# Kernel optimization log

Hardware: AMD Instinct MI355X
Metric: run time of the kernel (lower is better)

The kernel has to match this reference:

```python
import jax, jax.numpy as jnp
import numpy as np

EPS = 1e-12  # torch F.normalize eps

def _l2norm(x, axis):
    n = jnp.sqrt(jnp.sum(x * x, axis=axis, keepdims=True))
    return x / jnp.maximum(n, EPS)

def setup_inputs() -> dict:
    key = jax.random.key(0)
    k1, k2, k3, k4 = jax.random.split(key, 4)
    B, Lq, Ld, D, NWAY = 128, 32, 180, 128, 8
    query_reps = jax.random.normal(k1, (B, Lq, D), dtype=jnp.float32)
    doc_reps = jax.random.normal(k2, (B, NWAY, Ld, D), dtype=jnp.float32)
    doc_mask = jax.random.randint(k3, (B, NWAY, Ld), 0, 2, dtype=jnp.int32)
    # labels are teacher log-probabilities (KLDivLoss log_target=True)
    labels = jax.nn.log_softmax(jax.random.normal(k4, (B, NWAY), dtype=jnp.float32), axis=-1)
    return {"query_reps": query_reps, "doc_reps": doc_reps, "doc_mask": doc_mask, "labels": labels}

def reference(query_reps, doc_reps, doc_mask, labels):
    # query: L2-normalize over feature dim (dim=2 in torch call)
    q = _l2norm(query_reps, axis=-1)                      # [B, Lq, D]
    # docs: mask padding tokens, then F.normalize with DEFAULT dim=1,
    # i.e. L2-normalize along the token axis (faithful to source).
    d = doc_reps * doc_mask[..., None].astype(doc_reps.dtype)  # [B, W, Ld, D]
    d = _l2norm(d, axis=2)
    # MaxSim: sim[b,w,q,l] = <q_bq, d_bwl>; max over doc tokens, sum over query tokens
    sim = jnp.einsum('bqd,bwld->bwql', q, d)              # [B, W, Lq, Ld]
    scores = jnp.max(sim, axis=-1).sum(axis=-1)           # [B, W]
    log_p = jax.nn.log_softmax(scores, axis=-1)           # == log(softmax(scores))
    # KLDivLoss(log_target=True, reduction='batchmean'): sum(exp(t)*(t - x)) / B
    B = scores.shape[0]
    loss = jnp.sum(jnp.exp(labels) * (labels - log_p)) / B
    return loss  # torch.mean of a scalar is the scalar
```

## Files before the change

### kernel.cpp

```cpp
#include <hip/hip_runtime.h>
#include <math.h>
#include <stdint.h>

#define NB 128
#define LQ 32
#define LD 180
#define DD 128
#define NW 8
#define NBW (NB*NW)
#define PB 40
#define LROWS 192

typedef __attribute__((ext_vector_type(8)))  short short8v;
typedef __attribute__((ext_vector_type(16))) float f32x16;

static __device__ __forceinline__ void bar() {
    asm volatile("s_waitcnt lgkmcnt(0)" ::: "memory");
    __builtin_amdgcn_s_barrier();
}

static __device__ __forceinline__ void split2(float x, short& h, short& l) {
    uint32_t u = __float_as_uint(x);
    h = (short)(u >> 16);
    float r = x - __uint_as_float(u & 0xffff0000u);
    l = (short)(__float_as_uint(r) >> 16);
}

__global__ __launch_bounds__(512, 4) void maxsim_kernel(
    const float* __restrict__ qreps, const float* __restrict__ dreps,
    const int* __restrict__ dmask, float* __restrict__ scores)
{
    __shared__ short s_dh[LROWS * PB];
    __shared__ short s_dl[LROWS * PB];
    __shared__ short s_qh[LQ * PB];
    __shared__ short s_ql[LQ * PB];
    __shared__ float s_ssq[8 * 32];
    __shared__ float s_dinv[32];
    __shared__ float s_qinv[32];
    __shared__ float s_pm[6][LQ];

    const int t = threadIdx.x, bw = blockIdx.x, b = bw >> 3;
    const int lane = t & 63, wave = t >> 6;
    const int d4 = t & 7;
    const int rb = t >> 3;
    const int lh = lane >> 5, l31 = lane & 31;

    const float4* doc4 = (const float4*)(dreps + (size_t)bw * LD * DD);
    const float4* q4g  = (const float4*)(qreps + (size_t)b * LQ * DD);
    const int*    mrow = dmask + bw * LD;

    float4 dv0 = doc4[(rb      ) * 32 + d4];
    float4 dv1 = doc4[(rb + 64 ) * 32 + d4];
    float4 dv2;
    if (rb < 52) dv2 = doc4[(rb + 128) * 32 + d4];
    float4 qv, qn;
    if (t < 256) qv = q4g[(t >> 3) * 32 + d4];

    const float mk0 = (float)mrow[rb];
    const float mk1 = (float)mrow[rb + 64];
    const float mk2 = (rb < 52) ? (float)mrow[rb + 128] : 0.0f;

    {
        int r = t >> 4, sub = t & 15;
        float4 a = q4g[r * 32 + sub];
        float4 c = q4g[r * 32 + 16 + sub];
        float ss = a.x*a.x + a.y*a.y + a.z*a.z + a.w*a.w
                 + c.x*c.x + c.y*c.y + c.z*c.z + c.w*c.w;
        ss += __shfl_xor(ss, 8);
        ss += __shfl_xor(ss, 4);
        ss += __shfl_xor(ss, 2);
        ss += __shfl_xor(ss, 1);
        if (sub == 0) s_qinv[r] = 1.0f / fmaxf(sqrtf(ss), 1e-12f);
    }

    f32x16 acc = {};

    #pragma unroll
    for (int cc = 0; cc < 4; ++cc) {
        if (cc) bar();

        float4 pssq = make_float4(0.f, 0.f, 0.f, 0.f);
        {
            float4 v = dv0; float m = mk0;
            v.x *= m; v.y *= m; v.z *= m; v.w *= m;
            pssq.x += v.x*v.x; pssq.y += v.y*v.y; pssq.z += v.z*v.z; pssq.w += v.w*v.w;
            short4 h, lo;
            split2(v.x, h.x, lo.x); split2(v.y, h.y, lo.y);
            split2(v.z, h.z, lo.z); split2(v.w, h.w, lo.w);
            *(short4*)&s_dh[rb * PB + 4 * d4] = h;
            *(short4*)&s_dl[rb * PB + 4 * d4] = lo;
        }
        {
            float4 v = dv1; float m = mk1;
            v.x *= m; v.y *= m; v.z *= m; v.w *= m;
            pssq.x += v.x*v.x; pssq.y += v.y*v.y; pssq.z += v.z*v.z; pssq.w += v.w*v.w;
            short4 h, lo;
            split2(v.x, h.x, lo.x); split2(v.y, h.y, lo.y);
            split2(v.z, h.z, lo.z); split2(v.w, h.w, lo.w);
            *(short4*)&s_dh[(rb + 64) * PB + 4 * d4] = h;
            *(short4*)&s_dl[(rb + 64) * PB + 4 * d4] = lo;
        }
        if (rb < 52) {
            float4 v = dv2; float m = mk2;
            v.x *= m; v.y *= m; v.z *= m; v.w *= m;
            pssq.x += v.x*v.x; pssq.y += v.y*v.y; pssq.z += v.z*v.z; pssq.w += v.w*v.w;
            short4 h, lo;
            split2(v.x, h.x, lo.x); split2(v.y, h.y, lo.y);
            split2(v.z, h.z, lo.z); split2(v.w, h.w, lo.w);
            *(short4*)&s_dh[(rb + 128) * PB + 4 * d4] = h;
            *(short4*)&s_dl[(rb + 128) * PB + 4 * d4] = lo;
        } else if (cc == 0) {
            short4 z = make_short4(0, 0, 0, 0);
            *(short4*)&s_dh[(rb + 128) * PB + 4 * d4] = z;
            *(short4*)&s_dl[(rb + 128) * PB + 4 * d4] = z;
        }

        if (cc < 3) {
            dv0 = doc4[(rb      ) * 32 + (cc + 1) * 8 + d4];
            dv1 = doc4[(rb + 64 ) * 32 + (cc + 1) * 8 + d4];
            if (rb < 52) dv2 = doc4[(rb + 128) * 32 + (cc + 1) * 8 + d4];
            if (t < 256) qn = q4g[(t >> 3) * 32 + (cc + 1) * 8 + d4];
        }

        #pragma unroll
        for (int off = 8; off <= 32; off <<= 1) {
            pssq.x += __shfl_xor(pssq.x, off);
            pssq.y += __shfl_xor(pssq.y, off);
            pssq.z += __shfl_xor(pssq.z, off);
            pssq.w += __shfl_xor(pssq.w, off);
        }
        if (lane < 8) *(float4*)&s_ssq[wave * 32 + 4 * lane] = pssq;
        bar();

        if (t < 32) {
            float tot = 0.f;
            #pragma unroll
            for (int w = 0; w < 8; ++w) tot += s_ssq[w * 32 + t];
            s_dinv[t] = 1.0f / fmaxf(sqrtf(tot), 1e-12f);
        }
        bar();

        if (t < 256) {
            float qi = s_qinv[t >> 3];
            float4 di = *(const float4*)&s_dinv[4 * d4];
            float4 v = qv;
            v.x *= qi * di.x; v.y *= qi * di.y;
            v.z *= qi * di.z; v.w *= qi * di.w;
            short4 h, lo;
            split2(v.x, h.x, lo.x); split2(v.y, h.y, lo.y);
            split2(v.z, h.z, lo.z); split2(v.w, h.w, lo.w);
            *(short4*)&s_qh[(t >> 3) * PB + 4 * d4] = h;
            *(short4*)&s_ql[(t >> 3) * PB + 4 * d4] = lo;
        }
        if (cc < 3) qv = qn;
        bar();

        if (wave < 6) {
            #pragma unroll
            for (int kk = 0; kk < 2; ++kk) {
                int ao = l31 * PB + 16 * kk + 8 * lh;
                short8v ah = *(const short8v*)&s_qh[ao];
                short8v al = *(const short8v*)&s_ql[ao];
                int bo = (32 * wave + l31) * PB + 16 * kk + 8 * lh;
                short8v bh = *(const short8v*)&s_dh[bo];
                short8v bl = *(const short8v*)&s_dl[bo];
                acc = __builtin_amdgcn_mfma_f32_32x32x16_bf16(ah, bh, acc, 0, 0, 0);
                acc = __builtin_amdgcn_mfma_f32_32x32x16_bf16(ah, bl, acc, 0, 0, 0);
                acc = __builtin_amdgcn_mfma_f32_32x32x16_bf16(al, bh, acc, 0, 0, 0);
            }
        }
    }

    if (wave < 6) {
        float pm[16];
        #pragma unroll
        for (int r = 0; r < 16; ++r) pm[r] = acc[r];
        #pragma unroll
        for (int off = 1; off <= 16; off <<= 1)
            #pragma unroll
            for (int r = 0; r < 16; ++r)
                pm[r] = fmaxf(pm[r], __shfl_xor(pm[r], off));
        if (l31 == 0) {
            #pragma unroll
            for (int r = 0; r < 16; ++r)
                s_pm[wave][(r & 3) + 8 * (r >> 2) + 4 * lh] = pm[r];
        }
    }
    bar();
    if (t < 32) {
        float v = s_pm[0][t];
        #pragma unroll
        for (int w = 1; w < 6; ++w) v = fmaxf(v, s_pm[w][t]);
        #pragma unroll
        for (int off = 16; off >= 1; off >>= 1) v += __shfl_xor(v, off);
        if (t == 0) scores[bw] = v;
    }
}

__global__ __launch_bounds__(NB) void finish_kernel(
    const float* __restrict__ scores, const float* __restrict__ labels,
    float* __restrict__ out)
{
    __shared__ float s_part[2];
    const int t = threadIdx.x;
    const float* sr = scores + t * NW;
    const float* lr = labels + t * NW;

    float s[NW];
    float m = -INFINITY;
    #pragma unroll
    for (int w = 0; w < NW; ++w) { s[w] = sr[w]; m = fmaxf(m, s[w]); }
    float se = 0.f;
    #pragma unroll
    for (int w = 0; w < NW; ++w) se += expf(s[w] - m);
    float lse = logf(se) + m;

    float term = 0.f;
    #pragma unroll
    for (int w = 0; w < NW; ++w) {
        float lw = lr[w];
        term += expf(lw) * (lw - (s[w] - lse));
    }
    #pragma unroll
    for (int off = 32; off > 0; off >>= 1) term += __shfl_xor(term, off);
    if ((t & 63) == 0) s_part[t >> 6] = term;
    __syncthreads();
    if (t == 0) out[0] = (s_part[0] + s_part[1]) / (float)NB;
}

extern "C" void kernel_launch(void* const* d_in, const int* in_sizes, int n_in,
                              void* d_out, int out_size, void* d_ws, size_t ws_size,
                              hipStream_t stream) {
    const float* qreps  = (const float*)d_in[0];
    const float* dreps  = (const float*)d_in[1];
    const int*   dmask  = (const int*)d_in[2];
    const float* labels = (const float*)d_in[3];
    float* out = (float*)d_out;
    float* scores = (float*)d_ws;

    maxsim_kernel<<<NBW, 512, 0, stream>>>(qreps, dreps, dmask, scores);
    finish_kernel<<<1, NB, 0, stream>>>(scores, labels, out);
}
```

Baseline: 151.6 us.

## Double-buffer LDS stages and overlap query scaling with MFMA compute

Doubles the LDS buffers for doc and query hi/lo splits so the next 32-wide feature chunk is staged while the current chunk runs through MFMA. The two idle waves (6 and 7) now compute the per-column doc inverse norms and the scaled query split concurrently with the MFMA waves, which cuts barriers per chunk from three to two. The cost is roughly twice the shared memory, which may lower occupancy below the four blocks per CU requested in the launch bounds.

```diff
diff --git a/kernel.cpp b/kernel.cpp
--- a/kernel.cpp
+++ b/kernel.cpp
@@ -30,13 +30,13 @@
     const float* __restrict__ qreps, const float* __restrict__ dreps,
     const int* __restrict__ dmask, float* __restrict__ scores)
 {
-    __shared__ short s_dh[LROWS * PB];
-    __shared__ short s_dl[LROWS * PB];
-    __shared__ short s_qh[LQ * PB];
-    __shared__ short s_ql[LQ * PB];
-    __shared__ float s_ssq[8 * 32];
-    __shared__ float s_dinv[32];
-    __shared__ float s_qinv[32];
+    __shared__ short s_dh[2][LROWS * PB];
+    __shared__ short s_dl[2][LROWS * PB];
+    __shared__ short s_qh[2][LQ * PB];
+    __shared__ short s_ql[2][LQ * PB];
+    __shared__ float s_ssq[2][8][32];
+    __shared__ float s_dinv[2][2][32];
+    __shared__ float s_qinv[LQ];
     __shared__ float s_pm[6][LQ];
 
     const int t = threadIdx.x, bw = blockIdx.x, b = bw >> 3;
@@ -44,21 +44,23 @@
     const int d4 = t & 7;
     const int rb = t >> 3;
     const int lh = lane >> 5, l31 = lane & 31;
+    const bool has2 = (rb < 52);
 
     const float4* doc4 = (const float4*)(dreps + (size_t)bw * LD * DD);
     const float4* q4g  = (const float4*)(qreps + (size_t)b * LQ * DD);
     const int*    mrow = dmask + bw * LD;
 
-    float4 dv0 = doc4[(rb      ) * 32 + d4];
-    float4 dv1 = doc4[(rb + 64 ) * 32 + d4];
-    float4 dv2;
-    if (rb < 52) dv2 = doc4[(rb + 128) * 32 + d4];
-    float4 qv, qn;
-    if (t < 256) qv = q4g[(t >> 3) * 32 + d4];
+    float4 dv0 = doc4[rb * 32 + d4];
+    float4 dv1 = doc4[(rb + 64) * 32 + d4];
+    float4 dv2 = make_float4(0.f, 0.f, 0.f, 0.f);
+    if (has2) dv2 = doc4[(rb + 128) * 32 + d4];
+    float4 qv0;
+    if (t < 256) qv0 = q4g[rb * 32 + d4];
+    float4 qf0, qf1;
 
     const float mk0 = (float)mrow[rb];
     const float mk1 = (float)mrow[rb + 64];
-    const float mk2 = (rb < 52) ? (float)mrow[rb + 128] : 0.0f;
+    const float mk2 = has2 ? (float)mrow[rb + 128] : 0.0f;
 
     {
         int r = t >> 4, sub = t & 15;
@@ -72,103 +74,147 @@
         ss += __shfl_xor(ss, 1);
         if (sub == 0) s_qinv[r] = 1.0f / fmaxf(sqrtf(ss), 1e-12f);
     }
-
-    f32x16 acc = {};
-
-    #pragma unroll
-    for (int cc = 0; cc < 4; ++cc) {
-        if (cc) bar();
-
-        float4 pssq = make_float4(0.f, 0.f, 0.f, 0.f);
+    if (rb >= 52) {
+        short4 z = make_short4(0, 0, 0, 0);
+        int off = (rb + 128) * PB + 4 * d4;
+        *(short4*)&s_dh[0][off] = z; *(short4*)&s_dl[0][off] = z;
+        *(short4*)&s_dh[1][off] = z; *(short4*)&s_dl[1][off] = z;
+    }
+
+    auto stage = [&](short* dh, short* dl, float* ssqw,
+                     float4 a0, float4 a1, float4 a2) {
+        float4 ps = make_float4(0.f, 0.f, 0.f, 0.f);
         {
-            float4 v = dv0; float m = mk0;
-            v.x *= m; v.y *= m; v.z *= m; v.w *= m;
-            pssq.x += v.x*v.x; pssq.y += v.y*v.y; pssq.z += v.z*v.z; pssq.w += v.w*v.w;
+            float4 v = a0;
+            v.x *= mk0; v.y *= mk0; v.z *= mk0; v.w *= mk0;
+            ps.x += v.x*v.x; ps.y += v.y*v.y; ps.z += v.z*v.z; ps.w += v.w*v.w;
             short4 h, lo;
             split2(v.x, h.x, lo.x); split2(v.y, h.y, lo.y);
             split2(v.z, h.z, lo.z); split2(v.w, h.w, lo.w);
-            *(short4*)&s_dh[rb * PB + 4 * d4] = h;
-            *(short4*)&s_dl[rb * PB + 4 * d4] = lo;
+            *(short4*)&dh[rb * PB + 4 * d4] = h;
+            *(short4*)&dl[rb * PB + 4 * d4] = lo;
         }
         {
-            float4 v = dv1; float m = mk1;
-            v.x *= m; v.y *= m; v.z *= m; v.w *= m;
-            pssq.x += v.x*v.x; pssq.y += v.y*v.y; pssq.z += v.z*v.z; pssq.w += v.w*v.w;
+            float4 v = a1;
+            v.x *= mk1; v.y *= mk1; v.z *= mk1; v.w *= mk1;
+            ps.x += v.x*v.x; ps.y += v.y*v.y; ps.z += v.z*v.z; ps.w += v.w*v.w;
             short4 h, lo;
             split2(v.x, h.x, lo.x); split2(v.y, h.y, lo.y);
             split2(v.z, h.z, lo.z); split2(v.w, h.w, lo.w);
-            *(short4*)&s_dh[(rb + 64) * PB + 4 * d4] = h;
-            *(short4*)&s_dl[(rb + 64) * PB + 4 * d4] = lo;
-        }
-        if (rb < 52) {
-            float4 v = dv2; float m = mk2;
-            v.x *= m; v.y *= m; v.z *= m; v.w *= m;
-            pssq.x += v.x*v.x; pssq.y += v.y*v.y; pssq.z += v.z*v.z; pssq.w += v.w*v.w;
+            *(short4*)&dh[(rb + 64) * PB + 4 * d4] = h;
+            *(short4*)&dl[(rb + 64) * PB + 4 * d4] = lo;
+        }
+        if (has2) {
+            float4 v = a2;
+            v.x *= mk2; v.y *= mk2; v.z *= mk2; v.w *= mk2;
+            ps.x += v.x*v.x; ps.y += v.y*v.y; ps.z += v.z*v.z; ps.w += v.w*v.w;
             short4 h, lo;
             split2(v.x, h.x, lo.x); split2(v.y, h.y, lo.y);
             split2(v.z, h.z, lo.z); split2(v.w, h.w, lo.w);
-            *(short4*)&s_dh[(rb + 128) * PB + 4 * d4] = h;
-            *(short4*)&s_dl[(rb + 128) * PB + 4 * d4] = lo;
-        } else if (cc == 0) {
-            short4 z = make_short4(0, 0, 0, 0);
-            *(short4*)&s_dh[(rb + 128) * PB + 4 * d4] = z;
-            *(short4*)&s_dl[(rb + 128) * PB + 4 * d4] = z;
-        }
-
+            *(short4*)&dh[(rb + 128) * PB + 4 * d4] = h;
+            *(short4*)&dl[(rb + 128) * PB + 4 * d4] = lo;
+        }
+        #pragma unroll
+        for (int off = 8; off <= 32; off <<= 1) {
+            ps.x += __shfl_xor(ps.x, off);
+            ps.y += __shfl_xor(ps.y, off);
+            ps.z += __shfl_xor(ps.z, off);
+            ps.w += __shfl_xor(ps.w, off);
+        }
+        if (lane < 8) *(float4*)&ssqw[wave * 32 + 4 * lane] = ps;
+    };
+
+    stage(s_dh[0], s_dl[0], &s_ssq[0][0][0], dv0, dv1, dv2);
+    dv0 = doc4[rb * 32 + 8 + d4];
+    dv1 = doc4[(rb + 64) * 32 + 8 + d4];
+    if (has2) dv2 = doc4[(rb + 128) * 32 + 8 + d4];
+    bar();
+    if (t < 32) {
+        float tot = 0.f;
+        #pragma unroll
+        for (int w = 0; w < 8; ++w) tot += s_ssq[0][w][t];
+        s_dinv[0][0][t] = 1.0f / fmaxf(sqrtf(tot), 1e-12f);
+    }
+    bar();
+    if (t < 256) {
+        float qi = s_qinv[rb];
+        float4 dvec = *(const float4*)&s_dinv[0][0][4 * d4];
+        float4 v = qv0;
+        v.x *= qi * dvec.x; v.y *= qi * dvec.y;
+        v.z *= qi * dvec.z; v.w *= qi * dvec.w;
+        short4 h, lo;
+        split2(v.x, h.x, lo.x); split2(v.y, h.y, lo.y);
+        split2(v.z, h.z, lo.z); split2(v.w, h.w, lo.w);
+        *(short4*)&s_qh[0][rb * PB + 4 * d4] = h;
+        *(short4*)&s_ql[0][rb * PB + 4 * d4] = lo;
+    }
+    bar();
+
+    f32x16 acc = {};
+    #pragma unroll
+    for (int cc = 0; cc < 4; ++cc) {
+        const int Bc = cc & 1, Bn = Bc ^ 1;
         if (cc < 3) {
-            dv0 = doc4[(rb      ) * 32 + (cc + 1) * 8 + d4];
-            dv1 = doc4[(rb + 64 ) * 32 + (cc + 1) * 8 + d4];
-            if (rb < 52) dv2 = doc4[(rb + 128) * 32 + (cc + 1) * 8 + d4];
-            if (t < 256) qn = q4g[(t >> 3) * 32 + (cc + 1) * 8 + d4];
-        }
-
-        #pragma unroll
-        for (int off = 8; off <= 32; off <<= 1) {
-            pssq.x += __shfl_xor(pssq.x, off);
-            pssq.y += __shfl_xor(pssq.y, off);
-            pssq.z += __shfl_xor(pssq.z, off);
-            pssq.w += __shfl_xor(pssq.w, off);
-        }
-        if (lane < 8) *(float4*)&s_ssq[wave * 32 + 4 * lane] = pssq;
+            if (wave >= 6) {
+                int f = (wave - 6) * 64 + lane;
+                qf0 = q4g[(f >> 3) * 32 + (cc + 1) * 8 + (f & 7)];
+                qf1 = q4g[((f >> 3) + 16) * 32 + (cc + 1) * 8 + (f & 7)];
+            }
+            stage(s_dh[Bn], s_dl[Bn], &s_ssq[Bn][0][0], dv0, dv1, dv2);
+            if (cc < 2) {
+                dv0 = doc4[rb * 32 + (cc + 2) * 8 + d4];
+                dv1 = doc4[(rb + 64) * 32 + (cc + 2) * 8 + d4];
+                if (has2) dv2 = doc4[(rb + 128) * 32 + (cc + 2) * 8 + d4];
+            }
+        }
         bar();
-
-        if (t < 32) {
-            float tot = 0.f;
-            #pragma unroll
-            for (int w = 0; w < 8; ++w) tot += s_ssq[w * 32 + t];
-            s_dinv[t] = 1.0f / fmaxf(sqrtf(tot), 1e-12f);
-        }
-        bar();
-
-        if (t < 256) {
-            float qi = s_qinv[t >> 3];
-            float4 di = *(const float4*)&s_dinv[4 * d4];
-            float4 v = qv;
-            v.x *= qi * di.x; v.y *= qi * di.y;
-            v.z *= qi * di.z; v.w *= qi * di.w;
-            short4 h, lo;
-            split2(v.x, h.x, lo.x); split2(v.y, h.y, lo.y);
-            split2(v.z, h.z, lo.z); split2(v.w, h.w, lo.w);
-            *(short4*)&s_qh[(t >> 3) * PB + 4 * d4] = h;
-            *(short4*)&s_ql[(t >> 3) * PB + 4 * d4] = lo;
-        }
-        if (cc < 3) qv = qn;
-        bar();
-
         if (wave < 6) {
             #pragma unroll
             for (int kk = 0; kk < 2; ++kk) {
                 int ao = l31 * PB + 16 * kk + 8 * lh;
-                short8v ah = *(const short8v*)&s_qh[ao];
-                short8v al = *(const short8v*)&s_ql[ao];
+                short8v ah = *(const short8v*)&s_qh[Bc][ao];
+                short8v al = *(const short8v*)&s_ql[Bc][ao];
                 int bo = (32 * wave + l31) * PB + 16 * kk + 8 * lh;
-                short8v bh = *(const short8v*)&s_dh[bo];
-                short8v bl = *(const short8v*)&s_dl[bo];
+                short8v bh = *(const short8v*)&s_dh[Bc][bo];
+                short8v bl = *(const short8v*)&s_dl[Bc][bo];
                 acc = __builtin_amdgcn_mfma_f32_32x32x16_bf16(ah, bh, acc, 0, 0, 0);
                 acc = __builtin_amdgcn_mfma_f32_32x32x16_bf16(ah, bl, acc, 0, 0, 0);
                 acc = __builtin_amdgcn_mfma_f32_32x32x16_bf16(al, bh, acc, 0, 0, 0);
             }
-        }
+        } else if (cc < 3) {
+            const int w6 = wave - 6;
+            float tot = 0.f;
+            #pragma unroll
+            for (int w = 0; w < 8; ++w) tot += s_ssq[Bn][w][l31];
+            float di = 1.0f / fmaxf(sqrtf(tot), 1e-12f);
+            if (lane < 32) s_dinv[Bn][w6][l31] = di;
+            asm volatile("s_waitcnt lgkmcnt(0)" ::: "memory");
+            int f = w6 * 64 + lane;
+            int r0 = f >> 3, d4p = f & 7;
+            float4 dvec = *(const float4*)&s_dinv[Bn][w6][4 * d4p];
+            float qi0 = s_qinv[r0], qi1 = s_qinv[r0 + 16];
+            {
+                float4 v = qf0;
+                v.x *= qi0 * dvec.x; v.y *= qi0 * dvec.y;
+                v.z *= qi0 * dvec.z; v.w *= qi0 * dvec.w;
+                short4 h, lo;
+                split2(v.x, h.x, lo.x); split2(v.y, h.y, lo.y);
+                split2(v.z, h.z, lo.z); split2(v.w, h.w, lo.w);
+                *(short4*)&s_qh[Bn][r0 * PB + 4 * d4p] = h;
+                *(short4*)&s_ql[Bn][r0 * PB + 4 * d4p] = lo;
+            }
+            {
+                float4 v = qf1;
+                v.x *= qi1 * dvec.x; v.y *= qi1 * dvec.y;
+                v.z *= qi1 * dvec.z; v.w *= qi1 * dvec.w;
+                short4 h, lo;
+                split2(v.x, h.x, lo.x); split2(v.y, h.y, lo.y);
+                split2(v.z, h.z, lo.z); split2(v.w, h.w, lo.w);
+                *(short4*)&s_qh[Bn][(r0 + 16) * PB + 4 * d4p] = h;
+                *(short4*)&s_ql[Bn][(r0 + 16) * PB + 4 * d4p] = lo;
+            }
+        }
+        if (cc < 3) bar();
     }
 
     if (wave < 6) {
```

Result: no change. 153.5 us (+1.3%).
